# Performance work log

Measured on AMD Instinct MI355X. Metric: run time of the kernel, lower is better.

Reference implementation:

```python
import jax, jax.numpy as jnp
import numpy as np

N = 50000
NEG_SLOPE = 0.2


def gat_conv(x, src, dst, W, al, ar, b, activation):
    # x: [N, F_in]; W: [F_in, H*D]; al, ar: [H, D]; b: [H*D]
    H, D = al.shape
    f = (x @ W).reshape(N, H, D)                      # projected features [N,H,D]
    el = (f * al).sum(-1)                             # [N,H] source attention logits
    er = (f * ar).sum(-1)                             # [N,H] dest attention logits
    e = jax.nn.leaky_relu(el[src] + er[dst], NEG_SLOPE)   # [E,H]
    # edge softmax grouped by destination node
    emax = jax.ops.segment_max(e, dst, num_segments=N)    # [N,H]
    ee = jnp.exp(e - emax[dst])                            # [E,H]
    denom = jax.ops.segment_sum(ee, dst, num_segments=N)  # [N,H]
    alpha = ee / denom[dst]                                # [E,H]
    msg = f[src] * alpha[:, :, None]                       # [E,H,D]
    out = jax.ops.segment_sum(msg, dst, num_segments=N)   # [N,H,D]
    out = out + b.reshape(H, D)
    if activation is not None:
        out = activation(out)
    return out


def setup_inputs() -> dict:
    key = jax.random.key(0)
    ks = jax.random.split(key, 12)
    E = 800000
    F_in, Hid, Out = 128, 32, 32
    H1, H2 = 8, 1
    inputs = jax.random.normal(ks[0], (N, F_in), dtype=jnp.float32)
    src = jax.random.randint(ks[1], (E,), 0, N, dtype=jnp.int32)
    dst = jax.random.randint(ks[2], (E,), 0, N, dtype=jnp.int32)
    s1 = 1.0 / np.sqrt(F_in)
    s2 = 1.0 / np.sqrt(Hid * H1)
    W1 = jax.random.normal(ks[3], (F_in, H1 * Hid), dtype=jnp.float32) * s1
    al1 = jax.random.normal(ks[4], (H1, Hid), dtype=jnp.float32) * 0.1
    ar1 = jax.random.normal(ks[5], (H1, Hid), dtype=jnp.float32) * 0.1
    b1 = jnp.zeros((H1 * Hid,), dtype=jnp.float32)
    W2 = jax.random.normal(ks[6], (H1 * Hid, H2 * Out), dtype=jnp.float32) * s2
    al2 = jax.random.normal(ks[7], (H2, Out), dtype=jnp.float32) * 0.1
    ar2 = jax.random.normal(ks[8], (H2, Out), dtype=jnp.float32) * 0.1
    b2 = jnp.zeros((H2 * Out,), dtype=jnp.float32)
    return {"inputs": inputs, "src": src, "dst": dst,
            "W1": W1, "al1": al1, "ar1": ar1, "b1": b1,
            "W2": W2, "al2": al2, "ar2": ar2, "b2": b2}


def reference(inputs, src, dst, W1, al1, ar1, b1, W2, al2, ar2, b2):
    h = gat_conv(inputs, src, dst, W1, al1, ar1, b1, jax.nn.elu)  # [N,8,32]
    h = h.reshape(N, -1)                                          # flatten(1) -> [N,256]
    h = gat_conv(h, src, dst, W2, al2, ar2, b2, None)             # [N,1,32]
    return h.mean(1)                                              # [N,32]
```

## Files before the change

### kernel.cpp

```cpp
#include <hip/hip_runtime.h>
#include <math.h>

#define NEG_SLOPE 0.2f
#define CAP 64

typedef short v8s __attribute__((ext_vector_type(8)));
typedef float v4f __attribute__((ext_vector_type(4)));

__device__ inline unsigned short f2bf(float x) {
  unsigned u = __float_as_uint(x);
  u += 0x7fffu + ((u >> 16) & 1u);
  return (unsigned short)(u >> 16);
}

__device__ inline void acc8(float* a, uint4 v, float w) {
  a[0] += w * __uint_as_float(v.x << 16);
  a[1] += w * __uint_as_float(v.x & 0xffff0000u);
  a[2] += w * __uint_as_float(v.y << 16);
  a[3] += w * __uint_as_float(v.y & 0xffff0000u);
  a[4] += w * __uint_as_float(v.z << 16);
  a[5] += w * __uint_as_float(v.z & 0xffff0000u);
  a[6] += w * __uint_as_float(v.w << 16);
  a[7] += w * __uint_as_float(v.w & 0xffff0000u);
}

__device__ inline float lrelu_exp(float v) {
  v = (v >= 0.f) ? v : NEG_SLOPE * v;
  return __expf(v);
}

__global__ void k_fill(const int* __restrict__ src, const int* __restrict__ dst,
                       int* __restrict__ cnt, int* __restrict__ slots, int E,
                       const float* __restrict__ W1, unsigned short* __restrict__ W1T,
                       const float* __restrict__ W2, unsigned short* __restrict__ W2T) {
  int i = blockIdx.x * 256 + threadIdx.x;
  if (i < 32768) {
    int k = i & 127, nn = i >> 7;
    W1T[nn * 128 + k] = f2bf(W1[k * 256 + nn]);
  } else if (i < 32768 + 8192) {
    int g2 = i - 32768;
    int k = g2 & 255, c = g2 >> 8;
    W2T[c * 256 + k] = f2bf(W2[k * 32 + c]);
  }
  if (i < E) {
    int d = dst[i];
    int pos = atomicAdd(&cnt[d], 1);
    if (pos < CAP) slots[(size_t)d * CAP + pos] = src[i];
  }
}

__global__ __launch_bounds__(256) void k_gemm1(const float* __restrict__ x,
                                               const unsigned short* __restrict__ W1T,
                                               const float* __restrict__ al,
                                               const float* __restrict__ ar,
                                               unsigned short* __restrict__ f1b,
                                               float* __restrict__ el,
                                               float* __restrict__ er, int n) {
  __shared__ __align__(16) unsigned short xs[64][136];
  __shared__ __align__(16) unsigned short ws[64][136];
  const int tid = threadIdx.x;
  const int m0 = blockIdx.x * 64;

#pragma unroll
  for (int r = 0; r < 8; ++r) {
    int idx = r * 256 + tid;
    int m = idx >> 5, c4 = idx & 31;
    int gn = m0 + m;
    float4 v = make_float4(0.f, 0.f, 0.f, 0.f);
    if (gn < n) v = *(const float4*)(x + (size_t)gn * 128 + c4 * 4);
    ushort4 pk;
    pk.x = f2bf(v.x); pk.y = f2bf(v.y); pk.z = f2bf(v.z); pk.w = f2bf(v.w);
    *(ushort4*)(&xs[m][c4 * 4]) = pk;
  }

  const int wave = tid >> 6, lane = tid & 63;
  const int quad = lane >> 4, col16 = lane & 15;

  for (int cb = 0; cb < 4; ++cb) {
    const int c0 = cb * 64;
#pragma unroll
    for (int r = 0; r < 4; ++r) {
      int idx = r * 256 + tid;
      int m = idx >> 4, kc = idx & 15;
      const ushort4* q = (const ushort4*)(W1T + (size_t)(c0 + m) * 128 + kc * 8);
      *(ushort4*)(&ws[m][kc * 8]) = q[0];
      *(ushort4*)(&ws[m][kc * 8 + 4]) = q[1];
    }
    __syncthreads();

    v4f acc[4];
#pragma unroll
    for (int nt = 0; nt < 4; ++nt) acc[nt] = (v4f){0.f, 0.f, 0.f, 0.f};

#pragma unroll
    for (int kc = 0; kc < 4; ++kc) {
      v8s a = *(const v8s*)(&xs[wave * 16 + col16][kc * 32 + quad * 8]);
#pragma unroll
      for (int nt = 0; nt < 4; ++nt) {
        v8s b = *(const v8s*)(&ws[nt * 16 + col16][kc * 32 + quad * 8]);
        acc[nt] = __builtin_amdgcn_mfma_f32_16x16x32_bf16(a, b, acc[nt], 0, 0, 0);
      }
    }

    float pel[4][2], per_r[4][2];
#pragma unroll
    for (int rg = 0; rg < 4; ++rg) {
      pel[rg][0] = pel[rg][1] = 0.f;
      per_r[rg][0] = per_r[rg][1] = 0.f;
    }
#pragma unroll
    for (int nt = 0; nt < 4; ++nt) {
      int gcol = c0 + nt * 16 + col16;
      float alv = al[gcol], arv = ar[gcol];
      int hh = nt >> 1;
#pragma unroll
      for (int rg = 0; rg < 4; ++rg) {
        int gn = m0 + wave * 16 + quad * 4 + rg;
        float v = acc[nt][rg];
        if (gn < n) f1b[(size_t)gn * 256 + gcol] = f2bf(v);
        pel[rg][hh] += v * alv;
        per_r[rg][hh] += v * arv;
      }
    }
#pragma unroll
    for (int off = 1; off < 16; off <<= 1) {
#pragma unroll
      for (int rg = 0; rg < 4; ++rg) {
#pragma unroll
        for (int hh = 0; hh < 2; ++hh) {
          pel[rg][hh] += __shfl_xor(pel[rg][hh], off, 64);
          per_r[rg][hh] += __shfl_xor(per_r[rg][hh], off, 64);
        }
      }
    }
    if (col16 == 0) {
      int hb = cb * 2;
#pragma unroll
      for (int rg = 0; rg < 4; ++rg) {
        int gn = m0 + wave * 16 + quad * 4 + rg;
        if (gn < n) {
#pragma unroll
          for (int hh = 0; hh < 2; ++hh) {
            el[gn * 8 + hb + hh] = pel[rg][hh];
            er[gn * 8 + hb + hh] = per_r[rg][hh];
          }
        }
      }
    }
    __syncthreads();
  }
}

__global__ __launch_bounds__(256) void k_agg1(const unsigned short* __restrict__ f1b,
                                              const float* __restrict__ el,
                                              const float* __restrict__ er,
                                              const int* __restrict__ cnt,
                                              const int* __restrict__ slots,
                                              const float* __restrict__ b1,
                                              unsigned short* __restrict__ houtb, int n) {
  const int wv = threadIdx.x >> 6, lane = threadIdx.x & 63;
  const int node = blockIdx.x * 4 + wv;
  if (node >= n) return;
  const int h2 = lane >> 5, lane32 = lane & 31;
  const int hd = lane32 >> 2;
  const int start = node * CAP;
  const int deg = min(cnt[node], CAP);
  const float er0 = er[(size_t)node * 8 + hd];
  const int sv = slots[start + lane];

  float a[8];
#pragma unroll
  for (int d = 0; d < 8; ++d) a[d] = 0.f;
  float dw = 0.f;
  const unsigned short* fbase = f1b + lane32 * 8;

  for (int jb = 0; jb < deg; jb += 16) {
    const int j = jb + h2;
    int s[8];
    bool g[8];
    uint4 v[8];
    float e[8];
#pragma unroll
    for (int t = 0; t < 8; ++t) {
      s[t] = __shfl(sv, j + 2 * t, 64);
      g[t] = (j + 2 * t) < deg;
    }
#pragma unroll
    for (int t = 0; t < 8; ++t) {
      v[t] = make_uint4(0, 0, 0, 0);
      e[t] = 0.f;
      if (g[t]) {
        v[t] = *(const uint4*)(fbase + (size_t)s[t] * 256);
        e[t] = el[(size_t)s[t] * 8 + hd];
      }
    }
#pragma unroll
    for (int t = 0; t < 8; ++t) {
      if (g[t]) {
        float w = lrelu_exp(e[t] + er0);
        acc8(a, v[t], w);
        dw += w;
      }
    }
  }

#pragma unroll
  for (int d = 0; d < 8; ++d) a[d] += __shfl_xor(a[d], 32, 64);
  dw += __shfl_xor(dw, 32, 64);

  if (h2 == 0) {
    float inv = (deg > 0) ? 1.f / dw : 0.f;
    float4 b0 = *(const float4*)(b1 + lane32 * 8);
    float4 b4 = *(const float4*)(b1 + lane32 * 8 + 4);
    float o[8];
    o[0] = a[0] * inv + b0.x; o[1] = a[1] * inv + b0.y;
    o[2] = a[2] * inv + b0.z; o[3] = a[3] * inv + b0.w;
    o[4] = a[4] * inv + b4.x; o[5] = a[5] * inv + b4.y;
    o[6] = a[6] * inv + b4.z; o[7] = a[7] * inv + b4.w;
#pragma unroll
    for (int d = 0; d < 8; ++d) o[d] = (o[d] > 0.f) ? o[d] : (__expf(o[d]) - 1.f);
    uint4 pk;
    pk.x = (unsigned)f2bf(o[0]) | ((unsigned)f2bf(o[1]) << 16);
    pk.y = (unsigned)f2bf(o[2]) | ((unsigned)f2bf(o[3]) << 16);
    pk.z = (unsigned)f2bf(o[4]) | ((unsigned)f2bf(o[5]) << 16);
    pk.w = (unsigned)f2bf(o[6]) | ((unsigned)f2bf(o[7]) << 16);
    *(uint4*)(houtb + (size_t)node * 256 + lane32 * 8) = pk;
  }
}

__global__ __launch_bounds__(256) void k_gemm2(const unsigned short* __restrict__ hb,
                                               const unsigned short* __restrict__ W2T,
                                               const float* __restrict__ al2,
                                               const float* __restrict__ ar2,
                                               unsigned short* __restrict__ f2b,
                                               float* __restrict__ el2,
                                               float* __restrict__ er2, int n) {
  __shared__ __align__(16) unsigned short xs[64][264];
  __shared__ __align__(16) unsigned short ws[32][264];
  const int tid = threadIdx.x;
  const int m0 = blockIdx.x * 64;

#pragma unroll
  for (int r = 0; r < 8; ++r) {
    int idx = r * 256 + tid;
    int m = idx >> 5, kc = idx & 31;
    int gn = m0 + m;
    ushort4 a0 = make_ushort4(0, 0, 0, 0), a1 = a0;
    if (gn < n) {
      const ushort4* p = (const ushort4*)(hb + (size_t)gn * 256 + kc * 8);
      a0 = p[0]; a1 = p[1];
    }
    *(ushort4*)(&xs[m][kc * 8]) = a0;
    *(ushort4*)(&xs[m][kc * 8 + 4]) = a1;
  }
#pragma unroll
  for (int r = 0; r < 4; ++r) {
    int idx = r * 256 + tid;
    int m = idx >> 5, kc = idx & 31;
    const ushort4* q = (const ushort4*)(W2T + (size_t)m * 256 + kc * 8);
    *(ushort4*)(&ws[m][kc * 8]) = q[0];
    *(ushort4*)(&ws[m][kc * 8 + 4]) = q[1];
  }
  __syncthreads();

  const int wave = tid >> 6, lane = tid & 63;
  const int quad = lane >> 4, col16 = lane & 15;

  v4f acc[2];
  acc[0] = (v4f){0.f, 0.f, 0.f, 0.f};
  acc[1] = (v4f){0.f, 0.f, 0.f, 0.f};

#pragma unroll
  for (int kc = 0; kc < 8; ++kc) {
    v8s a = *(const v8s*)(&xs[wave * 16 + col16][kc * 32 + quad * 8]);
#pragma unroll
    for (int nt = 0; nt < 2; ++nt) {
      v8s b = *(const v8s*)(&ws[nt * 16 + col16][kc * 32 + quad * 8]);
      acc[nt] = __builtin_amdgcn_mfma_f32_16x16x32_bf16(a, b, acc[nt], 0, 0, 0);
    }
  }

  float pel[4], per_r[4];
#pragma unroll
  for (int rg = 0; rg < 4; ++rg) { pel[rg] = 0.f; per_r[rg] = 0.f; }
#pragma unroll
  for (int nt = 0; nt < 2; ++nt) {
    int gcol = nt * 16 + col16;
    float alv = al2[gcol], arv = ar2[gcol];
#pragma unroll
    for (int rg = 0; rg < 4; ++rg) {
      int gn = m0 + wave * 16 + quad * 4 + rg;
      float v = acc[nt][rg];
      if (gn < n) f2b[(size_t)gn * 32 + gcol] = f2bf(v);
      pel[rg] += v * alv;
      per_r[rg] += v * arv;
    }
  }
#pragma unroll
  for (int off = 1; off < 16; off <<= 1) {
#pragma unroll
    for (int rg = 0; rg < 4; ++rg) {
      pel[rg] += __shfl_xor(pel[rg], off, 64);
      per_r[rg] += __shfl_xor(per_r[rg], off, 64);
    }
  }
  if (col16 == 0) {
#pragma unroll
    for (int rg = 0; rg < 4; ++rg) {
      int gn = m0 + wave * 16 + quad * 4 + rg;
      if (gn < n) { el2[gn] = pel[rg]; er2[gn] = per_r[rg]; }
    }
  }
}

__global__ __launch_bounds__(256) void k_agg2(const unsigned short* __restrict__ f2b,
                                              const float* __restrict__ el2,
                                              const float* __restrict__ er2,
                                              const int* __restrict__ cnt,
                                              const int* __restrict__ slots,
                                              const float* __restrict__ b2,
                                              float* __restrict__ out, int n) {
  const int wid = threadIdx.x >> 6, lane = threadIdx.x & 63;
  const int node = blockIdx.x * 4 + wid;
  if (node >= n) return;
  const int g = lane >> 3, d2 = lane & 7;
  const int start = node * CAP;
  const int deg = min(cnt[node], CAP);
  const float er0 = er2[node];
  const int sv = slots[start + lane];

  float a[4] = {0.f, 0.f, 0.f, 0.f};
  float dw = 0.f;
  const unsigned short* fbase = f2b + d2 * 4;

  int s[8];
  bool c[8];
  uint2 v[8];
  float e[8];
#pragma unroll
  for (int t = 0; t < 8; ++t) {
    int j = g + 8 * t;
    s[t] = __shfl(sv, j, 64);
    c[t] = j < deg;
  }
#pragma unroll
  for (int t = 0; t < 8; ++t) {
    v[t] = make_uint2(0, 0);
    e[t] = 0.f;
    if (c[t]) {
      v[t] = *(const uint2*)(fbase + (size_t)s[t] * 32);
      e[t] = el2[s[t]];
    }
  }
#pragma unroll
  for (int t = 0; t < 8; ++t) {
    if (c[t]) {
      float w = lrelu_exp(e[t] + er0);
      a[0] += w * __uint_as_float(v[t].x << 16);
      a[1] += w * __uint_as_float(v[t].x & 0xffff0000u);
      a[2] += w * __uint_as_float(v[t].y << 16);
      a[3] += w * __uint_as_float(v[t].y & 0xffff0000u);
      dw += w;
    }
  }
#pragma unroll
  for (int off = 8; off <= 32; off <<= 1) {
#pragma unroll
    for (int d = 0; d < 4; ++d) a[d] += __shfl_xor(a[d], off, 64);
    dw += __shfl_xor(dw, off, 64);
  }
  if (g == 0) {
    float inv = (deg > 0) ? 1.f / dw : 0.f;
    float4 b = *(const float4*)(b2 + d2 * 4);
    float4 r;
    r.x = a[0] * inv + b.x;
    r.y = a[1] * inv + b.y;
    r.z = a[2] * inv + b.z;
    r.w = a[3] * inv + b.w;
    *(float4*)(out + (size_t)node * 32 + d2 * 4) = r;
  }
}


extern "C" void kernel_launch(void* const* d_in, const int* in_sizes, int n_in,
                              void* d_out, int out_size, void* d_ws, size_t ws_size,
                              hipStream_t stream) {
  const float* x   = (const float*)d_in[0];
  const int*   src = (const int*)d_in[1];
  const int*   dst = (const int*)d_in[2];
  const float* W1  = (const float*)d_in[3];
  const float* al1 = (const float*)d_in[4];
  const float* ar1 = (const float*)d_in[5];
  const float* b1  = (const float*)d_in[6];
  const float* W2  = (const float*)d_in[7];
  const float* al2 = (const float*)d_in[8];
  const float* ar2 = (const float*)d_in[9];
  const float* b2  = (const float*)d_in[10];
  float* out = (float*)d_out;

  int N = in_sizes[0] / 128;
  int E = in_sizes[1];

  char* w = (char*)d_ws;
  auto alloc = [&](size_t nbytes) -> void* {
    void* p = (void*)w;
    w += ((nbytes + 255) / 256) * 256;
    return p;
  };
  unsigned short* W1T = (unsigned short*)alloc(256 * 128 * 2);
  unsigned short* W2T = (unsigned short*)alloc(32 * 256 * 2);
  unsigned short* f1b = (unsigned short*)alloc((size_t)N * 256 * 2);
  unsigned short* hb  = (unsigned short*)alloc((size_t)N * 256 * 2);
  unsigned short* f2b = (unsigned short*)alloc((size_t)N * 32 * 2);
  float* el1  = (float*)alloc((size_t)N * 8 * 4);
  float* er1  = (float*)alloc((size_t)N * 8 * 4);
  float* el2  = (float*)alloc((size_t)N * 4);
  float* er2  = (float*)alloc((size_t)N * 4);
  int* cnt    = (int*)alloc((size_t)N * 4);
  int* slots  = (int*)alloc((size_t)N * CAP * 4);

  hipMemsetAsync(cnt, 0, (size_t)N * 4, stream);
  hipLaunchKernelGGL(k_fill, dim3((E + 255) / 256), dim3(256), 0, stream, src, dst, cnt, slots, E,
                     W1, W1T, W2, W2T);
  hipLaunchKernelGGL(k_gemm1, dim3((N + 63) / 64), dim3(256), 0, stream, x, W1T, al1, ar1, f1b, el1, er1, N);
  hipLaunchKernelGGL(k_agg1, dim3((N + 3) / 4), dim3(256), 0, stream, f1b, el1, er1, cnt, slots, b1, hb, N);
  hipLaunchKernelGGL(k_gemm2, dim3((N + 63) / 64), dim3(256), 0, stream, hb, W2T, al2, ar2, f2b, el2, er2, N);
  hipLaunchKernelGGL(k_agg2, dim3((N + 3) / 4), dim3(256), 0, stream, f2b, el2, er2, cnt, slots, b2, out, N);
}
```

Baseline: 254.0 us.

## Co-schedule edge bucketing with layer-1 GEMM in one launch

Moves the weight transpose/bf16 conversion into a small separate kernel, then merges the edge-slot fill and the layer-1 projection GEMM into a single grid. The first 512 blocks handle the edge atomics, each thread covering 8 edges with batched loads, while the remaining blocks run the GEMM. The goal is to let the latency-bound atomic scatter overlap with the compute-bound GEMM and to cut the number of threads doing atomics. The cost is an extra tiny launch for the weight prep, plus the risk that the fill blocks leave GEMM blocks waiting or uneven.

```diff
diff --git a/kernel.cpp b/kernel.cpp
--- a/kernel.cpp
+++ b/kernel.cpp
@@ -3,6 +3,7 @@
 
 #define NEG_SLOPE 0.2f
 #define CAP 64
+#define FILLB 512
 
 typedef short v8s __attribute__((ext_vector_type(8)));
 typedef float v4f __attribute__((ext_vector_type(4)));
@@ -29,10 +30,8 @@
   return __expf(v);
 }
 
-__global__ void k_fill(const int* __restrict__ src, const int* __restrict__ dst,
-                       int* __restrict__ cnt, int* __restrict__ slots, int E,
-                       const float* __restrict__ W1, unsigned short* __restrict__ W1T,
-                       const float* __restrict__ W2, unsigned short* __restrict__ W2T) {
+__global__ void k_prepw(const float* __restrict__ W1, unsigned short* __restrict__ W1T,
+                        const float* __restrict__ W2, unsigned short* __restrict__ W2T) {
   int i = blockIdx.x * 256 + threadIdx.x;
   if (i < 32768) {
     int k = i & 127, nn = i >> 7;
@@ -42,24 +41,45 @@
     int k = g2 & 255, c = g2 >> 8;
     W2T[c * 256 + k] = f2bf(W2[k * 32 + c]);
   }
-  if (i < E) {
-    int d = dst[i];
-    int pos = atomicAdd(&cnt[d], 1);
-    if (pos < CAP) slots[(size_t)d * CAP + pos] = src[i];
-  }
-}
-
-__global__ __launch_bounds__(256) void k_gemm1(const float* __restrict__ x,
+}
+
+__global__ __launch_bounds__(256) void k_fuse1(const int* __restrict__ src, const int* __restrict__ dst,
+                                               int* __restrict__ cnt, int* __restrict__ slots, int E,
                                                const unsigned short* __restrict__ W1T,
-                                               const float* __restrict__ al,
-                                               const float* __restrict__ ar,
+                                               const float* __restrict__ x,
+                                               const float* __restrict__ al, const float* __restrict__ ar,
                                                unsigned short* __restrict__ f1b,
-                                               float* __restrict__ el,
-                                               float* __restrict__ er, int n) {
+                                               float* __restrict__ el, float* __restrict__ er, int n) {
   __shared__ __align__(16) unsigned short xs[64][136];
   __shared__ __align__(16) unsigned short ws[64][136];
   const int tid = threadIdx.x;
-  const int m0 = blockIdx.x * 64;
+  const int bid = blockIdx.x;
+
+  if (bid < FILLB) {
+    const int t0 = bid * 256 + tid;
+    const int stride = FILLB * 256;
+    int d[8], sc[8];
+    bool valid[8];
+#pragma unroll
+    for (int k = 0; k < 8; ++k) {
+      int i = t0 + k * stride;
+      valid[k] = i < E;
+      d[k] = valid[k] ? dst[i] : 0;
+      sc[k] = valid[k] ? src[i] : 0;
+    }
+    int pos[8];
+#pragma unroll
+    for (int k = 0; k < 8; ++k) {
+      if (valid[k]) pos[k] = atomicAdd(&cnt[d[k]], 1);
+    }
+#pragma unroll
+    for (int k = 0; k < 8; ++k) {
+      if (valid[k] && pos[k] < CAP) slots[(size_t)d[k] * CAP + pos[k]] = sc[k];
+    }
+    return;
+  }
+
+  const int m0 = (bid - FILLB) * 64;
 
 #pragma unroll
   for (int r = 0; r < 8; ++r) {
@@ -420,9 +440,10 @@
   int* slots  = (int*)alloc((size_t)N * CAP * 4);
 
   hipMemsetAsync(cnt, 0, (size_t)N * 4, stream);
-  hipLaunchKernelGGL(k_fill, dim3((E + 255) / 256), dim3(256), 0, stream, src, dst, cnt, slots, E,
-                     W1, W1T, W2, W2T);
-  hipLaunchKernelGGL(k_gemm1, dim3((N + 63) / 64), dim3(256), 0, stream, x, W1T, al1, ar1, f1b, el1, er1, N);
+  hipLaunchKernelGGL(k_prepw, dim3(161), dim3(256), 0, stream, W1, W1T, W2, W2T);
+  hipLaunchKernelGGL(k_fuse1, dim3(FILLB + (N + 63) / 64), dim3(256), 0, stream,
+                     src, dst, cnt, slots, E, W1T,
+                     x, al1, ar1, f1b, el1, er1, N);
   hipLaunchKernelGGL(k_agg1, dim3((N + 3) / 4), dim3(256), 0, stream, f1b, el1, er1, cnt, slots, b1, hb, N);
   hipLaunchKernelGGL(k_gemm2, dim3((N + 63) / 64), dim3(256), 0, stream, hb, W2T, al2, ar2, f2b, el2, er2, N);
   hipLaunchKernelGGL(k_agg2, dim3((N + 3) / 4), dim3(256), 0, stream, f2b, el2, er2, cnt, slots, b2, out, N);
```

After: 247.5 us. 1.03x faster.
